# Kernel tuning notes

Measured on AMD Instinct MI355X. Metric: run time of the kernel, lower is better.

## Reference

```python
import jax, jax.numpy as jnp
import numpy as np

BETA = 0.25


def setup_inputs() -> dict:
    key = jax.random.key(0)
    k1, k2 = jax.random.split(key)
    x = jax.random.normal(k1, (64, 32, 32, 64), dtype=jnp.float32)
    # codebook stored as [embedding_dim, num_embeddings], as in the layer
    embeddings = jax.random.normal(k2, (64, 1024), dtype=jnp.float32) * 0.05
    return {"x": x, "embeddings": embeddings}


def reference(x, embeddings):
    input_shape = x.shape
    d = embeddings.shape[0]
    flat = x.reshape(-1, d)  # [N, D]

    sim = flat @ embeddings  # [N, K]
    distances = (
        jnp.sum(flat ** 2, axis=1, keepdims=True)
        + jnp.sum(embeddings ** 2, axis=0)
        - 2.0 * sim
    )
    encoding_indices = jnp.argmin(distances, axis=1)  # [N]

    # one_hot @ embeddings.T is mathematically a gather of codebook rows
    quantized = jnp.take(embeddings.T, encoding_indices, axis=0)  # [N, D]
    quantized = quantized.reshape(input_shape)

    commitment_loss = jnp.mean((jax.lax.stop_gradient(quantized) - x) ** 2)
    codebook_loss = jnp.mean((quantized - jax.lax.stop_gradient(x)) ** 2)
    loss = BETA * commitment_loss + codebook_loss

    # straight-through estimator
    quantized_st = x + jax.lax.stop_gradient(quantized - x)
    return quantized_st, loss
```

## Files before the change

### kernel.cpp

```cpp
#include <hip/hip_runtime.h>

#define D 64
#define K 1024
#define NPTS 65536
#define OUT_ELEMS (NPTS * D)
#define PAD4 17

typedef __bf16 bf16x8 __attribute__((ext_vector_type(8)));
typedef float  f32x4  __attribute__((ext_vector_type(4)));


static __device__ __forceinline__ void split1(float v, __bf16& h, __bf16& mid,
                                              __bf16& lo) {
    h = (__bf16)v;
    const float fh = (float)h;
    const float r1 = v - fh;
    mid = (__bf16)r1;
    const float fm = (float)mid;
    lo = (__bf16)(r1 - fm);
}

__global__ __launch_bounds__(256) void vq_prep(const float* __restrict__ emb,
                                               float* __restrict__ eT,
                                               float* __restrict__ enorm_h,
                                               __bf16* __restrict__ ebh,
                                               __bf16* __restrict__ ebm,
                                               __bf16* __restrict__ ebl,
                                               float* __restrict__ loss_out) {
    __shared__ float tile[64][65];
    const int t    = threadIdx.x;
    const int lane = t & 63;
    const int quad = t >> 6;
    const int k0   = blockIdx.x * 64;

#pragma unroll
    for (int i = 0; i < 16; ++i) {
        const int d = i * 4 + quad;
        tile[d][lane] = emb[d * K + k0 + lane];
    }
    __syncthreads();

    const int kk = t >> 2, c = t & 3;
    const int krow = k0 + kk;
#pragma unroll
    for (int j = 0; j < 16; ++j) {
        const int d = c * 16 + j;
        const float v = tile[d][kk];
        const int idx = krow * D + d;
        eT[idx] = v;
        __bf16 h, mid, lo;
        split1(v, h, mid, lo);
        ebh[idx] = h; ebm[idx] = mid; ebl[idx] = lo;
    }

    if (t < 64) {
        float s = __fmul_rn(tile[0][t], tile[0][t]);
        for (int dd = 1; dd < D; ++dd)
            s = __fadd_rn(s, __fmul_rn(tile[dd][t], tile[dd][t]));
        enorm_h[k0 + t] = 0.5f * s;
    }
    if (blockIdx.x == 0 && t == 0) *loss_out = 0.0f;
}

static __device__ __forceinline__ float sq8(float a, float b, float c, float d,
                                            float e, float f, float g, float h) {
    float r = __fmul_rn(a, a);
    r = __fadd_rn(r, __fmul_rn(b, b));
    r = __fadd_rn(r, __fmul_rn(c, c));
    r = __fadd_rn(r, __fmul_rn(d, d));
    r = __fadd_rn(r, __fmul_rn(e, e));
    r = __fadd_rn(r, __fmul_rn(f, f));
    r = __fadd_rn(r, __fmul_rn(g, g));
    r = __fadd_rn(r, __fmul_rn(h, h));
    return r;
}

#define PINF(v) asm volatile("" : "+v"(v))

#define MFMA(A, B, C) C = __builtin_amdgcn_mfma_f32_16x16x32_bf16(A, B, C, 0, 0, 0)

#define MKFRAG(FH, FM, FL, U0, U1) {                      \
    __bf16 h_, m_, l_;                                    \
    split1(U0.x, h_, m_, l_); FH[0]=h_; FM[0]=m_; FL[0]=l_; \
    split1(U0.y, h_, m_, l_); FH[1]=h_; FM[1]=m_; FL[1]=l_; \
    split1(U0.z, h_, m_, l_); FH[2]=h_; FM[2]=m_; FL[2]=l_; \
    split1(U0.w, h_, m_, l_); FH[3]=h_; FM[3]=m_; FL[3]=l_; \
    split1(U1.x, h_, m_, l_); FH[4]=h_; FM[4]=m_; FL[4]=l_; \
    split1(U1.y, h_, m_, l_); FH[5]=h_; FM[5]=m_; FL[5]=l_; \
    split1(U1.z, h_, m_, l_); FH[6]=h_; FM[6]=m_; FL[6]=l_; \
    split1(U1.w, h_, m_, l_); FH[7]=h_; FM[7]=m_; FL[7]=l_; }

static __device__ __forceinline__ void cp16(const void* gptr, void* lptr) {
    __builtin_amdgcn_global_load_lds(
        (const __attribute__((address_space(1))) void*)gptr,
        (__attribute__((address_space(3))) void*)lptr, 16, 0, 0);
}

__global__ __launch_bounds__(256, 2) void vq_main(const float* __restrict__ x,
        const float* __restrict__ eT, const float* __restrict__ enorm_h,
        const __bf16* __restrict__ ebh, const __bf16* __restrict__ ebm,
        const __bf16* __restrict__ ebl,
        float* __restrict__ out, float* __restrict__ loss_out) {
    __shared__ __align__(16) char smem[51712];
    float*  rpart = (float*)(smem + 12288);
    int*    swin  = (int*)(smem + 16384);
    float*  skey  = (float*)(smem + 16896);
    int*    sct   = (int*)(smem + 25088);
    float4* slab  = (float4*)(smem + 16896);

    const int t     = threadIdx.x;
    const int lane  = t & 63;
    const int w     = t >> 6;
    const int m     = lane & 15;
    const int quad  = lane >> 4;
    const int pbase = blockIdx.x * 128 + w * 32;

    const int n0   = lane >> 3;
    const int jj   = lane & 7;
    const int soff = n0 * 128 + (((jj - n0) & 7) << 4);
    const char* gsA = (w <= 1) ? (const char*)ebh : (const char*)ebm;
    const int   IA  = w & 1;
    const int   dA  = ((w <= 1) ? 0 : 2048) + IA * 1024;
    const int   sA  = soff + IA * 1024;
    const char* gsB = (const char*)ebl;
    const int   dB  = 4096 + w * 1024;
    const int   sB  = soff + w * 1024;

    const int o0 = (m * 8 + ((quad + m) & 7)) * 16;
    const int o1 = (m * 8 + ((4 + quad + m) & 7)) * 16;

    cp16(gsA + sA, smem + dA);
    if (w <= 1) cp16(gsB + sB, smem + dB);

    bf16x8 Ah00, Am00, Al00, Ah01, Am01, Al01;
    bf16x8 Ah10, Am10, Al10, Ah11, Am11, Al11;
#define LOADA(TT, HH, FH, FM, FL) {                                        \
    const float* px = x + ((size_t)(pbase + TT * 16 + m)) * D + HH * 32 + quad * 8; \
    const float4 u0 = *(const float4*)px;                                  \
    const float4 u1 = *(const float4*)(px + 4);                            \
    rpart[(w * 32 + TT * 16 + m) * 8 + (HH * 4 + quad)] =                  \
        sq8(u0.x, u0.y, u0.z, u0.w, u1.x, u1.y, u1.z, u1.w);               \
    MKFRAG(FH, FM, FL, u0, u1); }
    LOADA(0, 0, Ah00, Am00, Al00)
    LOADA(0, 1, Ah01, Am01, Al01)
    LOADA(1, 0, Ah10, Am10, Al10)
    LOADA(1, 1, Ah11, Am11, Al11)
#undef LOADA
    PINF(Ah00); PINF(Am00); PINF(Al00); PINF(Ah01); PINF(Am01); PINF(Al01);
    PINF(Ah10); PINF(Am10); PINF(Al10); PINF(Ah11); PINF(Am11); PINF(Al11);

    __syncthreads();

    const float FINF = 3.402823466e38f;
    float bk00 = FINF, bk01 = FINF, bk02 = FINF, bk03 = FINF;
    float bk10 = FINF, bk11 = FINF, bk12 = FINF, bk13 = FINF;
    int   bc00 = 0, bc01 = 0, bc02 = 0, bc03 = 0;
    int   bc10 = 0, bc11 = 0, bc12 = 0, bc13 = 0;

    for (int ct = 0; ct < 64; ++ct) {
        const int ctn = (ct + 1) & 63;
        const int nb  = ((ct + 1) & 1) * 6144;
        cp16(gsA + (size_t)ctn * 2048 + sA, smem + nb + dA);
        if (w <= 1) cp16(gsB + (size_t)ctn * 2048 + sB, smem + nb + dB);

        const float enh = enorm_h[ct * 16 + m];

        const char* bb = smem + (ct & 1) * 6144;
        const bf16x8 Bh0 = *(const bf16x8*)(bb + o0);
        const bf16x8 Bh1 = *(const bf16x8*)(bb + o1);
        const bf16x8 Bm0 = *(const bf16x8*)(bb + 2048 + o0);
        const bf16x8 Bm1 = *(const bf16x8*)(bb + 2048 + o1);
        const bf16x8 Bl0 = *(const bf16x8*)(bb + 4096 + o0);
        const bf16x8 Bl1 = *(const bf16x8*)(bb + 4096 + o1);

        f32x4 c0 = {0.f, 0.f, 0.f, 0.f};
        f32x4 c1 = {0.f, 0.f, 0.f, 0.f};
        MFMA(Ah00, Bh0, c0); MFMA(Ah10, Bh0, c1);
        MFMA(Ah01, Bh1, c0); MFMA(Ah11, Bh1, c1);
        MFMA(Am00, Bh0, c0); MFMA(Am10, Bh0, c1);
        MFMA(Am01, Bh1, c0); MFMA(Am11, Bh1, c1);
        MFMA(Ah00, Bm0, c0); MFMA(Ah10, Bm0, c1);
        MFMA(Ah01, Bm1, c0); MFMA(Ah11, Bm1, c1);
        MFMA(Am00, Bm0, c0); MFMA(Am10, Bm0, c1);
        MFMA(Am01, Bm1, c0); MFMA(Am11, Bm1, c1);
        MFMA(Ah00, Bl0, c0); MFMA(Ah10, Bl0, c1);
        MFMA(Ah01, Bl1, c0); MFMA(Ah11, Bl1, c1);
        MFMA(Al00, Bh0, c0); MFMA(Al10, Bh0, c1);
        MFMA(Al01, Bh1, c0); MFMA(Al11, Bh1, c1);

        { const float kv = enh - c0[0]; if (kv < bk00) { bk00 = kv; bc00 = ct; } }
        { const float kv = enh - c0[1]; if (kv < bk01) { bk01 = kv; bc01 = ct; } }
        { const float kv = enh - c0[2]; if (kv < bk02) { bk02 = kv; bc02 = ct; } }
        { const float kv = enh - c0[3]; if (kv < bk03) { bk03 = kv; bc03 = ct; } }
        { const float kv = enh - c1[0]; if (kv < bk10) { bk10 = kv; bc10 = ct; } }
        { const float kv = enh - c1[1]; if (kv < bk11) { bk11 = kv; bc11 = ct; } }
        { const float kv = enh - c1[2]; if (kv < bk12) { bk12 = kv; bc12 = ct; } }
        { const float kv = enh - c1[3]; if (kv < bk13) { bk13 = kv; bc13 = ct; } }

        __syncthreads();
    }

#define PUTC(TT, REG, BK, BC) {                                   \
    const int ploc = w * 32 + TT * 16 + quad * 4 + REG;           \
    skey[ploc * 16 + m] = BK; sct[ploc * 16 + m] = BC; }
    PUTC(0, 0, bk00, bc00) PUTC(0, 1, bk01, bc01)
    PUTC(0, 2, bk02, bc02) PUTC(0, 3, bk03, bc03)
    PUTC(1, 0, bk10, bc10) PUTC(1, 1, bk11, bc11)
    PUTC(1, 2, bk12, bc12) PUTC(1, 3, bk13, bc13)
#undef PUTC
    __syncthreads();

    if (t < 128) {
        const int p = t;
        const float* rp = rpart + p * 8;
        const float A = ((rp[0] + rp[1]) + (rp[2] + rp[3])) +
                        ((rp[4] + rp[5]) + (rp[6] + rp[7]));
        float fb = FINF;
        int   fi = 0;
#pragma unroll
        for (int c = 0; c < 16; ++c) {
            const float kv = skey[p * 16 + c];
            const int   iv = sct[p * 16 + c] * 16 + c;
            if (kv < fb || (kv == fb && iv < fi)) { fb = kv; fi = iv; }
        }
        swin[p] = fi;
        float lp = fmaf(2.0f, fb, A);
#pragma unroll
        for (int off = 32; off > 0; off >>= 1) lp += __shfl_down(lp, off, 64);
        if (lane == 0) atomicAdd(loss_out, lp * (1.25f / (float)OUT_ELEMS));
    }
    __syncthreads();

    {
        const int p = t >> 1, c = t & 1;
        const int fi = swin[p];
        const float4* qr = (const float4*)(eT + (size_t)fi * D) + c * 8;
        float4* dst = slab + p * PAD4 + c * 8;
#pragma unroll
        for (int j = 0; j < 8; ++j) dst[j] = qr[j];
    }
    __syncthreads();
    float4* og = (float4*)out + (size_t)blockIdx.x * 2048;
#pragma unroll
    for (int s = 0; s < 8; ++s) {
        const int f = s * 256 + t;
        og[f] = slab[(f >> 4) * PAD4 + (f & 15)];
    }
}

extern "C" void kernel_launch(void* const* d_in, const int* in_sizes, int n_in,
                              void* d_out, int out_size, void* d_ws, size_t ws_size,
                              hipStream_t stream) {
    const float* x   = (const float*)d_in[0];
    const float* emb = (const float*)d_in[1];
    float* out       = (float*)d_out;
    char*  ws        = (char*)d_ws;
    float*  eT       = (float*)ws;
    float*  enorm_h  = (float*)(ws + 262144);
    __bf16* ebh      = (__bf16*)(ws + 266240);
    __bf16* ebm      = (__bf16*)(ws + 397312);
    __bf16* ebl      = (__bf16*)(ws + 528384);
    float* loss_out  = out + OUT_ELEMS;

    vq_prep<<<dim3(K / 64), dim3(256), 0, stream>>>(emb, eT, enorm_h, ebh, ebm,
                                                    ebl, loss_out);
    vq_main<<<dim3(NPTS / 128), dim3(256), 0, stream>>>(x, eT, enorm_h, ebh,
                                                        ebm, ebl, out, loss_out);
}
```

Baseline: 125.0 us.

## Unroll codebook loop by two and split MFMA accumulators into independent chains

The codebook tile loop is unrolled by two so the double-buffer offsets become compile-time constants, and the barrier moves to the top of each tile. Each tile now reads its B fragments from shared memory before issuing the async prefetch into the other buffer, with a sched_barrier to hold that order. Each point tile's MFMA chain is split into two accumulators that are summed at the end, shortening the dependent chain. The aim is better overlap of loads and matrix ops and fewer MFMA dependency stalls, at the cost of more registers and a slightly different float summation order.

```diff
diff --git a/kernel.cpp b/kernel.cpp
--- a/kernel.cpp
+++ b/kernel.cpp
@@ -149,56 +149,58 @@
     PINF(Ah00); PINF(Am00); PINF(Al00); PINF(Ah01); PINF(Am01); PINF(Al01);
     PINF(Ah10); PINF(Am10); PINF(Al10); PINF(Ah11); PINF(Am11); PINF(Al11);
 
-    __syncthreads();
-
     const float FINF = 3.402823466e38f;
     float bk00 = FINF, bk01 = FINF, bk02 = FINF, bk03 = FINF;
     float bk10 = FINF, bk11 = FINF, bk12 = FINF, bk13 = FINF;
     int   bc00 = 0, bc01 = 0, bc02 = 0, bc03 = 0;
     int   bc10 = 0, bc11 = 0, bc12 = 0, bc13 = 0;
 
-    for (int ct = 0; ct < 64; ++ct) {
-        const int ctn = (ct + 1) & 63;
-        const int nb  = ((ct + 1) & 1) * 6144;
-        cp16(gsA + (size_t)ctn * 2048 + sA, smem + nb + dA);
-        if (w <= 1) cp16(gsB + (size_t)ctn * 2048 + sB, smem + nb + dB);
-
-        const float enh = enorm_h[ct * 16 + m];
-
-        const char* bb = smem + (ct & 1) * 6144;
-        const bf16x8 Bh0 = *(const bf16x8*)(bb + o0);
-        const bf16x8 Bh1 = *(const bf16x8*)(bb + o1);
-        const bf16x8 Bm0 = *(const bf16x8*)(bb + 2048 + o0);
-        const bf16x8 Bm1 = *(const bf16x8*)(bb + 2048 + o1);
-        const bf16x8 Bl0 = *(const bf16x8*)(bb + 4096 + o0);
-        const bf16x8 Bl1 = *(const bf16x8*)(bb + 4096 + o1);
-
-        f32x4 c0 = {0.f, 0.f, 0.f, 0.f};
-        f32x4 c1 = {0.f, 0.f, 0.f, 0.f};
-        MFMA(Ah00, Bh0, c0); MFMA(Ah10, Bh0, c1);
-        MFMA(Ah01, Bh1, c0); MFMA(Ah11, Bh1, c1);
-        MFMA(Am00, Bh0, c0); MFMA(Am10, Bh0, c1);
-        MFMA(Am01, Bh1, c0); MFMA(Am11, Bh1, c1);
-        MFMA(Ah00, Bm0, c0); MFMA(Ah10, Bm0, c1);
-        MFMA(Ah01, Bm1, c0); MFMA(Ah11, Bm1, c1);
-        MFMA(Am00, Bm0, c0); MFMA(Am10, Bm0, c1);
-        MFMA(Am01, Bm1, c0); MFMA(Am11, Bm1, c1);
-        MFMA(Ah00, Bl0, c0); MFMA(Ah10, Bl0, c1);
-        MFMA(Ah01, Bl1, c0); MFMA(Ah11, Bl1, c1);
-        MFMA(Al00, Bh0, c0); MFMA(Al10, Bh0, c1);
-        MFMA(Al01, Bh1, c0); MFMA(Al11, Bh1, c1);
-
-        { const float kv = enh - c0[0]; if (kv < bk00) { bk00 = kv; bc00 = ct; } }
-        { const float kv = enh - c0[1]; if (kv < bk01) { bk01 = kv; bc01 = ct; } }
-        { const float kv = enh - c0[2]; if (kv < bk02) { bk02 = kv; bc02 = ct; } }
-        { const float kv = enh - c0[3]; if (kv < bk03) { bk03 = kv; bc03 = ct; } }
-        { const float kv = enh - c1[0]; if (kv < bk10) { bk10 = kv; bc10 = ct; } }
-        { const float kv = enh - c1[1]; if (kv < bk11) { bk11 = kv; bc11 = ct; } }
-        { const float kv = enh - c1[2]; if (kv < bk12) { bk12 = kv; bc12 = ct; } }
-        { const float kv = enh - c1[3]; if (kv < bk13) { bk13 = kv; bc13 = ct; } }
-
-        __syncthreads();
-    }
+#define TILE_BODY(BBOFF, CT, PRET, PREOFF) {                               \
+    __syncthreads();             \
+    const char* bb = smem + (BBOFF);                                       \
+    const bf16x8 Bh0 = *(const bf16x8*)(bb + o0);                          \
+    const bf16x8 Bh1 = *(const bf16x8*)(bb + o1);                          \
+    const bf16x8 Bm0 = *(const bf16x8*)(bb + 2048 + o0);                   \
+    const bf16x8 Bm1 = *(const bf16x8*)(bb + 2048 + o1);                   \
+    const bf16x8 Bl0 = *(const bf16x8*)(bb + 4096 + o0);                   \
+    const bf16x8 Bl1 = *(const bf16x8*)(bb + 4096 + o1);                   \
+    cp16(gsA + (size_t)(PRET) * 2048 + sA, smem + (PREOFF) + dA);          \
+    if (w <= 1) cp16(gsB + (size_t)(PRET) * 2048 + sB, smem + (PREOFF) + dB); \
+    __builtin_amdgcn_sched_barrier(0);                \
+    const float enh = enorm_h[(CT) * 16 + m];                              \
+    f32x4 c0a = {0.f,0.f,0.f,0.f}, c0b = {0.f,0.f,0.f,0.f};                \
+    f32x4 c1a = {0.f,0.f,0.f,0.f}, c1b = {0.f,0.f,0.f,0.f};                \
+    MFMA(Ah00, Bh0, c0a); MFMA(Ah10, Bh0, c1a);                            \
+    MFMA(Ah01, Bh1, c0b); MFMA(Ah11, Bh1, c1b);                            \
+    MFMA(Am00, Bh0, c0a); MFMA(Am10, Bh0, c1a);                            \
+    MFMA(Am01, Bh1, c0b); MFMA(Am11, Bh1, c1b);                            \
+    MFMA(Ah00, Bm0, c0a); MFMA(Ah10, Bm0, c1a);                            \
+    MFMA(Ah01, Bm1, c0b); MFMA(Ah11, Bm1, c1b);                            \
+    MFMA(Am00, Bm0, c0a); MFMA(Am10, Bm0, c1a);                            \
+    MFMA(Am01, Bm1, c0b); MFMA(Am11, Bm1, c1b);                            \
+    MFMA(Ah00, Bl0, c0a); MFMA(Ah10, Bl0, c1a);                            \
+    MFMA(Ah01, Bl1, c0b); MFMA(Ah11, Bl1, c1b);                            \
+    MFMA(Al00, Bh0, c0a); MFMA(Al10, Bh0, c1a);                            \
+    MFMA(Al01, Bh1, c0b); MFMA(Al11, Bh1, c1b);                            \
+    const f32x4 c0 = c0a + c0b;                                            \
+    const f32x4 c1 = c1a + c1b;                                            \
+    { const float kv = enh - c0[0]; if (kv < bk00) { bk00 = kv; bc00 = (CT); } } \
+    { const float kv = enh - c0[1]; if (kv < bk01) { bk01 = kv; bc01 = (CT); } } \
+    { const float kv = enh - c0[2]; if (kv < bk02) { bk02 = kv; bc02 = (CT); } } \
+    { const float kv = enh - c0[3]; if (kv < bk03) { bk03 = kv; bc03 = (CT); } } \
+    { const float kv = enh - c1[0]; if (kv < bk10) { bk10 = kv; bc10 = (CT); } } \
+    { const float kv = enh - c1[1]; if (kv < bk11) { bk11 = kv; bc11 = (CT); } } \
+    { const float kv = enh - c1[2]; if (kv < bk12) { bk12 = kv; bc12 = (CT); } } \
+    { const float kv = enh - c1[3]; if (kv < bk13) { bk13 = kv; bc13 = (CT); } } }
+
+    for (int j = 0; j < 32; ++j) {
+        const int ct0 = 2 * j;
+        const int ct1 = 2 * j + 1;
+        const int tp2 = (2 * j + 2) & 63;
+        TILE_BODY(0,    ct0, ct1, 6144)
+        TILE_BODY(6144, ct1, tp2, 0)
+    }
+#undef TILE_BODY
 
 #define PUTC(TT, REG, BK, BC) {                                   \
     const int ploc = w * 32 + TT * 16 + quad * 4 + REG;           \
```

New measurement: 123.5 us. Within noise of the previous version (-1.2%).
